# Kernel optimization log

Measured on AMD Instinct MI355X. Metric: run time of the kernel, lower is better.

Reference implementation:

```python
import jax, jax.numpy as jnp
import numpy as np

B, S, DIM, H = 4, 2048, 1024, 16
DEPTH = DIM // H


def setup_inputs() -> dict:
    key = jax.random.key(0)
    ks = jax.random.split(key, 12)
    s = 0.02
    return {
        "Q": jax.random.normal(ks[0], (B, S, DIM), jnp.float32),
        "K": jax.random.normal(ks[1], (B, S, DIM), jnp.float32),
        "V": jax.random.normal(ks[2], (B, S, DIM), jnp.float32),
        "mask": jax.random.randint(ks[3], (B, 1, 1, S), 0, 2).astype(jnp.float32),
        "Wq": jax.random.normal(ks[4], (DIM, DIM), jnp.float32) * s,
        "bq": jnp.zeros((DIM,), jnp.float32),
        "Wk": jax.random.normal(ks[5], (DIM, DIM), jnp.float32) * s,
        "bk": jnp.zeros((DIM,), jnp.float32),
        "Wv": jax.random.normal(ks[6], (DIM, DIM), jnp.float32) * s,
        "bv": jnp.zeros((DIM,), jnp.float32),
        "Wo": jax.random.normal(ks[7], (DIM, DIM), jnp.float32) * s,
        "bo": jnp.zeros((DIM,), jnp.float32),
    }


def _split_heads(x):
    # [B,S,DIM] -> [B,H,S,DEPTH]
    return x.reshape(x.shape[0], x.shape[1], H, DEPTH).transpose(0, 2, 1, 3)


def reference(Q, K, V, mask, Wq, bq, Wk, bk, Wv, bv, Wo, bo):
    q = _split_heads(Q @ Wq + bq)
    k = _split_heads(K @ Wk + bk)
    v = _split_heads(V @ Wv + bv)
    # scaled dot-product attention; note original scales by sqrt(depth) = last dim of K after split
    logits = jnp.einsum("bhqd,bhkd->bhqk", q, k) / jnp.sqrt(jnp.float32(DEPTH))
    logits = logits + mask * -1e9
    attn = jax.nn.softmax(logits, axis=-1)
    ctx = jnp.einsum("bhqk,bhkd->bhqd", attn, v)
    ctx = ctx.transpose(0, 2, 1, 3).reshape(Q.shape[0], Q.shape[1], DIM)
    return ctx @ Wo + bo
```

## Files before the change

### kernel.cpp

```cpp
#include <hip/hip_runtime.h>

typedef short s16x8 __attribute__((ext_vector_type(8)));
typedef short s16x4 __attribute__((ext_vector_type(4)));
typedef float f32x4 __attribute__((ext_vector_type(4)));

#define MFMA32(a, b, c) __builtin_amdgcn_mfma_f32_16x16x32_bf16((a), (b), (c), 0, 0, 0)

__device__ __forceinline__ void stage16(const unsigned short* g, unsigned short* l) {
#if defined(__HIP_DEVICE_COMPILE__)
  __builtin_amdgcn_global_load_lds((const __attribute__((address_space(1))) unsigned int*)g,
                                   (__attribute__((address_space(3))) unsigned int*)l, 16, 0, 0);
#endif
}

__device__ __forceinline__ unsigned short f2b(float f) {
  unsigned int u = __builtin_bit_cast(unsigned int, f);
  unsigned int r = u + 0x7FFFu + ((u >> 16) & 1u);
  return (unsigned short)(r >> 16);
}
__device__ __forceinline__ unsigned int pk2(float a, float b) {
#if defined(__HIP_DEVICE_COMPILE__)
  unsigned int ua = __builtin_bit_cast(unsigned int, a);
  unsigned int ub = __builtin_bit_cast(unsigned int, b);
  ua += 0x7FFFu + ((ua >> 16) & 1u);
  ub += 0x7FFFu + ((ub >> 16) & 1u);
  return __builtin_amdgcn_perm(ub, ua, 0x07060302u);
#else
  return (unsigned int)f2b(a) | ((unsigned int)f2b(b) << 16);
#endif
}
__device__ __forceinline__ float fast_exp2(float x) {
#if defined(__HIP_DEVICE_COMPILE__) && __has_builtin(__builtin_amdgcn_exp2f)
  return __builtin_amdgcn_exp2f(x);
#else
  return exp2f(x);
#endif
}

__global__ void wtrans(const float* __restrict__ W0, const float* __restrict__ W1,
                       const float* __restrict__ W2, const float* __restrict__ W3,
                       unsigned short* __restrict__ T0, unsigned short* __restrict__ T1,
                       unsigned short* __restrict__ T2, unsigned short* __restrict__ T3) {
  const float* W;
  unsigned short* T;
  switch (blockIdx.z) {
    case 0: W = W0; T = T0; break;
    case 1: W = W1; T = T1; break;
    case 2: W = W2; T = T2; break;
    default: W = W3; T = T3; break;
  }
  __shared__ float tile[32][33];
  const int n0 = blockIdx.x << 5;
  const int k0 = blockIdx.y << 5;
  const int tx = threadIdx.x;
  const int ty = threadIdx.y;
#pragma unroll
  for (int j = 0; j < 4; ++j)
    tile[ty + 8 * j][tx] = W[(size_t)(k0 + ty + 8 * j) * 1024 + n0 + tx];
  __syncthreads();
#pragma unroll
  for (int j = 0; j < 4; ++j)
    T[(size_t)(n0 + ty + 8 * j) * 1024 + k0 + tx] = f2b(tile[tx][ty + 8 * j]);
}

__global__ __launch_bounds__(256, 3) void gemm_qkv(
    const float* __restrict__ Qf, const float* __restrict__ Kf, const float* __restrict__ Vf,
    const unsigned short* __restrict__ Wqt, const unsigned short* __restrict__ Wkt,
    const unsigned short* __restrict__ Wvt, const float* __restrict__ bq,
    const float* __restrict__ bk, const float* __restrict__ bv,
    unsigned short* __restrict__ qh, unsigned short* __restrict__ kh,
    unsigned short* __restrict__ vtb, float qscale) {
  const int lid = blockIdx.x + (blockIdx.y << 3) + (blockIdx.z << 9);
  const int xcd = lid & 7;
  const int s = lid >> 3;
  const int tx = s & 7;
  const int g = ((s >> 3) << 3) | xcd;
  const int ty = g & 63;
  const int tz = g >> 6;

  const float* A;
  const unsigned short* Bt;
  const float* bias;
  unsigned short* Cout;
  float oscale = 1.0f;
  int vmode = 0;
  switch (tz) {
    case 0: A = Qf; Bt = Wqt; bias = bq; Cout = qh; oscale = qscale; break;
    case 1: A = Kf; Bt = Wkt; bias = bk; Cout = kh; break;
    default: A = Vf; Bt = Wvt; bias = bv; Cout = vtb; vmode = 1; break;
  }
  __shared__ __align__(16) unsigned short As[2 * 128 * 32];
  __shared__ __align__(16) unsigned short Bs[2 * 128 * 32];
  const int n0 = tx * 128;
  const int m0 = ty * 128;
  const int tid = threadIdx.x;
  const int w = tid >> 6;
  const int lane = tid & 63;
  const int lr = lane & 15;
  const int lg = lane >> 4;
  const int wm = (w >> 1) << 6;
  const int wn = (w & 1) << 6;

  const int srow = w * 16 + (lane >> 2);
  const int sseg = lane & 3;
  const float* Ag0 = A + (size_t)(m0 + srow) * 1024 + sseg * 8;
  const float* Ag1 = A + (size_t)(m0 + 64 + srow) * 1024 + sseg * 8;
  const unsigned short* Bg0 = Bt + (size_t)(n0 + srow) * 1024 + sseg * 8;
  const unsigned short* Bg1 = Bt + (size_t)(n0 + 64 + srow) * 1024 + sseg * 8;
  unsigned short* Bl0 = &Bs[(w * 16) * 32];
  unsigned short* Bl1 = &Bs[(64 + w * 16) * 32];
  const int aoff0 = (w * 16) * 32 + lane * 8;
  const int aoff1 = (64 + w * 16) * 32 + lane * 8;

  f32x4 acc[4][4];
#pragma unroll
  for (int i = 0; i < 4; ++i)
#pragma unroll
    for (int j = 0; j < 4; ++j) {
      f32x4 z = {0.f, 0.f, 0.f, 0.f};
      acc[i][j] = z;
    }

  {
    float4 a0lo = *(const float4*)Ag0;
    float4 a0hi = *(const float4*)(Ag0 + 4);
    float4 a1lo = *(const float4*)Ag1;
    float4 a1hi = *(const float4*)(Ag1 + 4);
    stage16(Bg0, Bl0);
    stage16(Bg1, Bl1);
    uint4 u0, u1;
    u0.x = pk2(a0lo.x, a0lo.y); u0.y = pk2(a0lo.z, a0lo.w);
    u0.z = pk2(a0hi.x, a0hi.y); u0.w = pk2(a0hi.z, a0hi.w);
    u1.x = pk2(a1lo.x, a1lo.y); u1.y = pk2(a1lo.z, a1lo.w);
    u1.z = pk2(a1hi.x, a1hi.y); u1.w = pk2(a1hi.z, a1hi.w);
    *(uint4*)&As[aoff0] = u0;
    *(uint4*)&As[aoff1] = u1;
  }
  asm volatile("s_waitcnt vmcnt(0) lgkmcnt(0)\n\ts_barrier" ::: "memory");

  int cur = 0;
  for (int k0 = 0; k0 < 1024; k0 += 32) {
    const bool next = (k0 + 32) < 1024;
    float4 a0lo, a0hi, a1lo, a1hi;
    if (next) {
      a0lo = *(const float4*)(Ag0 + k0 + 32);
      a0hi = *(const float4*)(Ag0 + k0 + 36);
      a1lo = *(const float4*)(Ag1 + k0 + 32);
      a1hi = *(const float4*)(Ag1 + k0 + 36);
      const int nb = (cur ^ 1) * 4096;
      stage16(Bg0 + k0 + 32, Bl0 + nb);
      stage16(Bg1 + k0 + 32, Bl1 + nb);
    }
    const int cb = cur * 4096;
    s16x8 af[4], bfr[4];
#pragma unroll
    for (int mt = 0; mt < 4; ++mt)
      af[mt] = *(const s16x8*)&As[cb + (wm + mt * 16 + lr) * 32 + lg * 8];
#pragma unroll
    for (int nt = 0; nt < 4; ++nt)
      bfr[nt] = *(const s16x8*)&Bs[cb + (wn + nt * 16 + lr) * 32 + lg * 8];
#pragma unroll
    for (int mt = 0; mt < 4; ++mt)
#pragma unroll
      for (int nt = 0; nt < 4; ++nt)
        acc[mt][nt] = MFMA32(af[mt], bfr[nt], acc[mt][nt]);
    if (next) {
      const int nb = (cur ^ 1) * 4096;
      uint4 u0, u1;
      u0.x = pk2(a0lo.x, a0lo.y); u0.y = pk2(a0lo.z, a0lo.w);
      u0.z = pk2(a0hi.x, a0hi.y); u0.w = pk2(a0hi.z, a0hi.w);
      u1.x = pk2(a1lo.x, a1lo.y); u1.y = pk2(a1lo.z, a1lo.w);
      u1.z = pk2(a1hi.x, a1hi.y); u1.w = pk2(a1hi.z, a1hi.w);
      *(uint4*)&As[nb + aoff0] = u0;
      *(uint4*)&As[nb + aoff1] = u1;
    }
    asm volatile("s_waitcnt vmcnt(0) lgkmcnt(0)\n\ts_barrier" ::: "memory");
    cur ^= 1;
  }

  float bcol[4];
#pragma unroll
  for (int nt = 0; nt < 4; ++nt) bcol[nt] = bias[n0 + wn + nt * 16 + lr];

  if (vmode == 0) {
#pragma unroll
    for (int mt = 0; mt < 4; ++mt)
#pragma unroll
      for (int nt = 0; nt < 4; ++nt)
#pragma unroll
        for (int r = 0; r < 4; ++r) {
          float v = (acc[mt][nt][r] + bcol[nt]) * oscale;
          int row = m0 + wm + mt * 16 + lg * 4 + r;
          int col = n0 + wn + nt * 16 + lr;
          int b = row >> 11, ss = row & 2047, hh = col >> 6, d = col & 63;
          Cout[(((size_t)(b * 16 + hh) * 2048 + ss) << 6) + d] = f2b(v);
        }
  } else {
#pragma unroll
    for (int mt = 0; mt < 4; ++mt)
#pragma unroll
      for (int nt = 0; nt < 4; ++nt)
#pragma unroll
        for (int r = 0; r < 4; ++r) {
          float v = acc[mt][nt][r] + bcol[nt];
          int row = m0 + wm + mt * 16 + lg * 4 + r;
          int col = n0 + wn + nt * 16 + lr;
          int b = row >> 11, ss = row & 2047, hh = col >> 6, d = col & 63;
          Cout[(((size_t)(b * 16 + hh) * 64 + d) << 11) + ss] = f2b(v);
        }
  }
}

__global__ __launch_bounds__(256, 3) void gemm_out(const unsigned short* __restrict__ A,
                                                   const unsigned short* __restrict__ Bt,
                                                   const float* __restrict__ bias,
                                                   float* __restrict__ Cout) {
  const int lid = blockIdx.x + (blockIdx.y << 3);
  const int xcd = lid & 7;
  const int s = lid >> 3;
  const int tx = s & 7;
  const int ty = ((s >> 3) << 3) | xcd;

  __shared__ __align__(16) unsigned short As[2 * 128 * 32];
  __shared__ __align__(16) unsigned short Bs[2 * 128 * 32];
  const int n0 = tx * 128;
  const int m0 = ty * 128;
  const int tid = threadIdx.x;
  const int w = tid >> 6;
  const int lane = tid & 63;
  const int lr = lane & 15;
  const int lg = lane >> 4;
  const int wm = (w >> 1) << 6;
  const int wn = (w & 1) << 6;

  const int srow = w * 16 + (lane >> 2);
  const int sseg = lane & 3;
  const unsigned short* Ag0 = A + (size_t)(m0 + srow) * 1024 + sseg * 8;
  const unsigned short* Ag1 = A + (size_t)(m0 + 64 + srow) * 1024 + sseg * 8;
  const unsigned short* Bg0 = Bt + (size_t)(n0 + srow) * 1024 + sseg * 8;
  const unsigned short* Bg1 = Bt + (size_t)(n0 + 64 + srow) * 1024 + sseg * 8;
  unsigned short* Al0 = &As[(w * 16) * 32];
  unsigned short* Al1 = &As[(64 + w * 16) * 32];
  unsigned short* Bl0 = &Bs[(w * 16) * 32];
  unsigned short* Bl1 = &Bs[(64 + w * 16) * 32];

  f32x4 acc[4][4];
#pragma unroll
  for (int i = 0; i < 4; ++i)
#pragma unroll
    for (int j = 0; j < 4; ++j) {
      f32x4 z = {0.f, 0.f, 0.f, 0.f};
      acc[i][j] = z;
    }

  stage16(Ag0, Al0);
  stage16(Ag1, Al1);
  stage16(Bg0, Bl0);
  stage16(Bg1, Bl1);
  asm volatile("s_waitcnt vmcnt(0)\n\ts_barrier" ::: "memory");

  int cur = 0;
  for (int k0 = 0; k0 < 1024; k0 += 32) {
    if (k0 + 32 < 1024) {
      const int nb = (cur ^ 1) * 4096;
      stage16(Ag0 + k0 + 32, Al0 + nb);
      stage16(Ag1 + k0 + 32, Al1 + nb);
      stage16(Bg0 + k0 + 32, Bl0 + nb);
      stage16(Bg1 + k0 + 32, Bl1 + nb);
    }
    const int cb = cur * 4096;
    s16x8 af[4], bfr[4];
#pragma unroll
    for (int mt = 0; mt < 4; ++mt)
      af[mt] = *(const s16x8*)&As[cb + (wm + mt * 16 + lr) * 32 + lg * 8];
#pragma unroll
    for (int nt = 0; nt < 4; ++nt)
      bfr[nt] = *(const s16x8*)&Bs[cb + (wn + nt * 16 + lr) * 32 + lg * 8];
#pragma unroll
    for (int mt = 0; mt < 4; ++mt)
#pragma unroll
      for (int nt = 0; nt < 4; ++nt)
        acc[mt][nt] = MFMA32(af[mt], bfr[nt], acc[mt][nt]);
    asm volatile("s_waitcnt vmcnt(0)\n\ts_barrier" ::: "memory");
    cur ^= 1;
  }

  float bcol[4];
#pragma unroll
  for (int nt = 0; nt < 4; ++nt) bcol[nt] = bias[n0 + wn + nt * 16 + lr];

#pragma unroll
  for (int mt = 0; mt < 4; ++mt)
#pragma unroll
    for (int nt = 0; nt < 4; ++nt)
#pragma unroll
      for (int r = 0; r < 4; ++r) {
        float v = acc[mt][nt][r] + bcol[nt];
        int row = m0 + wm + mt * 16 + lg * 4 + r;
        int col = n0 + wn + nt * 16 + lr;
        Cout[(size_t)row * 1024 + col] = v;
      }
}

__global__ __launch_bounds__(256, 4) void flash_attn(const unsigned short* __restrict__ qh,
                                                     const unsigned short* __restrict__ kh,
                                                     const unsigned short* __restrict__ vt,
                                                     const float* __restrict__ mask,
                                                     unsigned short* __restrict__ ctx) {
  const float c2 = 1.4426950408889634e9f;
  const int id = blockIdx.x;
  const int bh = id & 63;
  const int qtile = id >> 6;
  const int b = bh >> 4;
  const int h = bh & 15;
  const int q0 = qtile << 7;
  const int tid = threadIdx.x;
  const int w = tid >> 6;
  const int lane = tid & 63;
  const int lr = lane & 15;
  const int lg = lane >> 4;

  __shared__ __align__(16) unsigned short Ks[2 * 64 * 64];
  __shared__ __align__(16) unsigned short Vs[2 * 64 * 64];

  const unsigned short* qbase = qh + ((size_t)bh * 2048 + q0 + w * 32) * 64;
  const unsigned short* kbase = kh + (size_t)bh * 2048 * 64;
  const unsigned short* vbase = vt + (size_t)bh * 64 * 2048;
  const float* mbase = mask + b * 2048;

  const int rowc = lane >> 3;
  const int gseg = (lane & 7) ^ rowc;
  const unsigned short* kg0 = kbase + (size_t)(w * 16 + rowc) * 64 + gseg * 8;
  const unsigned short* kg1 = kbase + (size_t)(w * 16 + 8 + rowc) * 64 + gseg * 8;
  const unsigned short* vg0 = vbase + (size_t)(w * 16 + rowc) * 2048 + gseg * 8;
  const unsigned short* vg1 = vbase + (size_t)(w * 16 + 8 + rowc) * 2048 + gseg * 8;
  unsigned short* kl0 = &Ks[(w * 16 + 0) * 64];
  unsigned short* kl1 = &Ks[(w * 16 + 8) * 64];
  unsigned short* vl0 = &Vs[(w * 16 + 0) * 64];
  unsigned short* vl1 = &Vs[(w * 16 + 8) * 64];

  s16x8 qf[2][2];
#pragma unroll
  for (int qt = 0; qt < 2; ++qt)
#pragma unroll
    for (int kk = 0; kk < 2; ++kk)
      qf[qt][kk] = *(const s16x8*)(qbase + (qt * 16 + lr) * 64 + kk * 32 + lg * 8);

  const s16x8 ones8 = {(short)0x3F80, (short)0x3F80, (short)0x3F80, (short)0x3F80,
                       (short)0x3F80, (short)0x3F80, (short)0x3F80, (short)0x3F80};

  f32x4 o_acc[2][4];
  f32x4 l_acc[2];
#pragma unroll
  for (int qt = 0; qt < 2; ++qt) {
    f32x4 z = {0.f, 0.f, 0.f, 0.f};
    l_acc[qt] = z;
#pragma unroll
    for (int dt = 0; dt < 4; ++dt) o_acc[qt][dt] = z;
  }

  stage16(kg0, kl0);
  stage16(kg1, kl1);
  stage16(vg0, vl0);
  stage16(vg1, vl1);
  asm volatile("s_waitcnt vmcnt(0)\n\ts_barrier" ::: "memory");

  int cur = 0;
  for (int t0 = 0; t0 < 2048; t0 += 64) {
    if (t0 + 64 < 2048) {
      const int nb = (cur ^ 1) * 4096;
      stage16(kg0 + (size_t)(t0 + 64) * 64, kl0 + nb);
      stage16(kg1 + (size_t)(t0 + 64) * 64, kl1 + nb);
      stage16(vg0 + (t0 + 64), vl0 + nb);
      stage16(vg1 + (t0 + 64), vl1 + nb);
    }
    float4 mk[4];
#pragma unroll
    for (int kt = 0; kt < 4; ++kt) mk[kt] = *(const float4*)(mbase + t0 + kt * 16 + lg * 4);

    const int cb = cur * 4096;
    const int sw = lr & 7;
    unsigned int pw[4][2][2];
#pragma unroll
    for (int kt = 0; kt < 4; ++kt) {
      const int krow = kt * 16 + lr;
      s16x8 kf0 = *(const s16x8*)&Ks[cb + krow * 64 + ((lg ^ sw) * 8)];
      s16x8 kf1 = *(const s16x8*)&Ks[cb + krow * 64 + (((4 + lg) ^ sw) * 8)];
      float ml0 = mk[kt].x * c2, ml1 = mk[kt].y * c2;
      float ml2 = mk[kt].z * c2, ml3 = mk[kt].w * c2;
#pragma unroll
      for (int qt = 0; qt < 2; ++qt) {
        f32x4 s = {0.f, 0.f, 0.f, 0.f};
        s = MFMA32(kf0, qf[qt][0], s);
        s = MFMA32(kf1, qf[qt][1], s);
        pw[kt][qt][0] = pk2(fast_exp2(s[0] - ml0), fast_exp2(s[1] - ml1));
        pw[kt][qt][1] = pk2(fast_exp2(s[2] - ml2), fast_exp2(s[3] - ml3));
      }
    }

#pragma unroll
    for (int c = 0; c < 2; ++c) {
      s16x8 pb[2];
#pragma unroll
      for (int qt = 0; qt < 2; ++qt) {
        uint4 u;
        u.x = pw[2 * c][qt][0];
        u.y = pw[2 * c][qt][1];
        u.z = pw[2 * c + 1][qt][0];
        u.w = pw[2 * c + 1][qt][1];
        pb[qt] = __builtin_bit_cast(s16x8, u);
        l_acc[qt] = MFMA32(ones8, pb[qt], l_acc[qt]);
      }
      const int plo = ((c << 2) | (lg >> 1)) ^ sw;
      const int phi = ((c << 2) | 2 | (lg >> 1)) ^ sw;
      const int sub = (lg & 1) * 4;
#pragma unroll
      for (int dt = 0; dt < 4; ++dt) {
        const int d = dt * 16 + lr;
        s16x4 vlo = *(const s16x4*)&Vs[cb + d * 64 + plo * 8 + sub];
        s16x4 vhi = *(const s16x4*)&Vs[cb + d * 64 + phi * 8 + sub];
        s16x8 vf = __builtin_shufflevector(vlo, vhi, 0, 1, 2, 3, 4, 5, 6, 7);
#pragma unroll
        for (int qt = 0; qt < 2; ++qt) o_acc[qt][dt] = MFMA32(vf, pb[qt], o_acc[qt][dt]);
      }
    }

    asm volatile("s_waitcnt vmcnt(0)\n\ts_barrier" ::: "memory");
    cur ^= 1;
  }

#pragma unroll
  for (int qt = 0; qt < 2; ++qt) {
    float inv = 1.0f / l_acc[qt][0];
    int q = q0 + w * 32 + qt * 16 + lr;
    unsigned short* cp = ctx + ((size_t)(b * 2048 + q) * 16 + h) * 64 + lg * 4;
#pragma unroll
    for (int dt = 0; dt < 4; ++dt) {
      f32x4 o = o_acc[qt][dt];
      uint2 u;
      u.x = pk2(o[0] * inv, o[1] * inv);
      u.y = pk2(o[2] * inv, o[3] * inv);
      *(uint2*)(cp + dt * 16) = u;
    }
  }
}

extern "C" void kernel_launch(void* const* d_in, const int* in_sizes, int n_in,
                              void* d_out, int out_size, void* d_ws, size_t ws_size,
                              hipStream_t stream) {
  (void)in_sizes; (void)n_in; (void)out_size; (void)ws_size;
  const float* Q = (const float*)d_in[0];
  const float* K = (const float*)d_in[1];
  const float* V = (const float*)d_in[2];
  const float* mask = (const float*)d_in[3];
  const float* Wq = (const float*)d_in[4];
  const float* bq = (const float*)d_in[5];
  const float* Wk = (const float*)d_in[6];
  const float* bk = (const float*)d_in[7];
  const float* Wv = (const float*)d_in[8];
  const float* bv = (const float*)d_in[9];
  const float* Wo = (const float*)d_in[10];
  const float* bo = (const float*)d_in[11];

  char* ws = (char*)d_ws;
  unsigned short* wqt = (unsigned short*)(ws + (size_t)0);
  unsigned short* wkt = (unsigned short*)(ws + ((size_t)2 << 20));
  unsigned short* wvt = (unsigned short*)(ws + ((size_t)4 << 20));
  unsigned short* wot = (unsigned short*)(ws + ((size_t)6 << 20));
  unsigned short* qhb = (unsigned short*)(ws + ((size_t)8 << 20));
  unsigned short* khb = (unsigned short*)(ws + ((size_t)24 << 20));
  unsigned short* vtb = (unsigned short*)(ws + ((size_t)40 << 20));
  unsigned short* ctx = (unsigned short*)(ws + ((size_t)56 << 20));

  wtrans<<<dim3(32, 32, 4), dim3(32, 8), 0, stream>>>(Wq, Wk, Wv, Wo, wqt, wkt, wvt, wot);

  const float qscale = 0.18033688011112042f;

  gemm_qkv<<<dim3(8, 64, 3), dim3(256), 0, stream>>>(Q, K, V, wqt, wkt, wvt, bq, bk, bv,
                                                     qhb, khb, vtb, qscale);

  flash_attn<<<dim3(1024), dim3(256), 0, stream>>>(qhb, khb, vtb, mask, ctx);

  gemm_out<<<dim3(8, 64), dim3(256), 0, stream>>>(ctx, wot, bo, (float*)d_out);
}
```

Before: 368.5 us.

## Triple-buffer LDS staging in projection GEMMs with two-deep prefetch

```diff
diff --git a/kernel.cpp b/kernel.cpp
--- a/kernel.cpp
+++ b/kernel.cpp
@@ -72,9 +72,9 @@
     unsigned short* __restrict__ vtb, float qscale) {
   const int lid = blockIdx.x + (blockIdx.y << 3) + (blockIdx.z << 9);
   const int xcd = lid & 7;
-  const int s = lid >> 3;
-  const int tx = s & 7;
-  const int g = ((s >> 3) << 3) | xcd;
+  const int sl = lid >> 3;
+  const int tx = sl & 7;
+  const int g = ((sl >> 3) << 3) | xcd;
   const int ty = g & 63;
   const int tz = g >> 6;
 
@@ -89,8 +89,8 @@
     case 1: A = Kf; Bt = Wkt; bias = bk; Cout = kh; break;
     default: A = Vf; Bt = Wvt; bias = bv; Cout = vtb; vmode = 1; break;
   }
-  __shared__ __align__(16) unsigned short As[2 * 128 * 32];
-  __shared__ __align__(16) unsigned short Bs[2 * 128 * 32];
+  __shared__ __align__(16) unsigned short As[3 * 128 * 32];
+  __shared__ __align__(16) unsigned short Bs[3 * 128 * 32];
   const int n0 = tx * 128;
   const int m0 = ty * 128;
   const int tid = threadIdx.x;
@@ -107,8 +107,10 @@
   const float* Ag1 = A + (size_t)(m0 + 64 + srow) * 1024 + sseg * 8;
   const unsigned short* Bg0 = Bt + (size_t)(n0 + srow) * 1024 + sseg * 8;
   const unsigned short* Bg1 = Bt + (size_t)(n0 + 64 + srow) * 1024 + sseg * 8;
-  unsigned short* Bl0 = &Bs[(w * 16) * 32];
-  unsigned short* Bl1 = &Bs[(64 + w * 16) * 32];
+  unsigned short *ab0 = &As[0], *ab1 = &As[4096], *ab2 = &As[8192];
+  unsigned short *bb0 = &Bs[0], *bb1 = &Bs[4096], *bb2 = &Bs[8192];
+  const int bl0 = (w * 16) * 32;
+  const int bl1 = (64 + w * 16) * 32;
   const int aoff0 = (w * 16) * 32 + lane * 8;
   const int aoff1 = (64 + w * 16) * 32 + lane * 8;
 
@@ -121,61 +123,68 @@
       acc[i][j] = z;
     }
 
+  float4 pa0lo, pa0hi, pa1lo, pa1hi;
+
+  stage16(Bg0, bb0 + bl0);
+  stage16(Bg1, bb0 + bl1);
+  stage16(Bg0 + 32, bb1 + bl0);
+  stage16(Bg1 + 32, bb1 + bl1);
+  pa0lo = *(const float4*)Ag0;
+  pa0hi = *(const float4*)(Ag0 + 4);
+  pa1lo = *(const float4*)Ag1;
+  pa1hi = *(const float4*)(Ag1 + 4);
   {
-    float4 a0lo = *(const float4*)Ag0;
-    float4 a0hi = *(const float4*)(Ag0 + 4);
-    float4 a1lo = *(const float4*)Ag1;
-    float4 a1hi = *(const float4*)(Ag1 + 4);
-    stage16(Bg0, Bl0);
-    stage16(Bg1, Bl1);
     uint4 u0, u1;
-    u0.x = pk2(a0lo.x, a0lo.y); u0.y = pk2(a0lo.z, a0lo.w);
-    u0.z = pk2(a0hi.x, a0hi.y); u0.w = pk2(a0hi.z, a0hi.w);
-    u1.x = pk2(a1lo.x, a1lo.y); u1.y = pk2(a1lo.z, a1lo.w);
-    u1.z = pk2(a1hi.x, a1hi.y); u1.w = pk2(a1hi.z, a1hi.w);
-    *(uint4*)&As[aoff0] = u0;
-    *(uint4*)&As[aoff1] = u1;
-  }
-  asm volatile("s_waitcnt vmcnt(0) lgkmcnt(0)\n\ts_barrier" ::: "memory");
-
-  int cur = 0;
-  for (int k0 = 0; k0 < 1024; k0 += 32) {
-    const bool next = (k0 + 32) < 1024;
-    float4 a0lo, a0hi, a1lo, a1hi;
-    if (next) {
-      a0lo = *(const float4*)(Ag0 + k0 + 32);
-      a0hi = *(const float4*)(Ag0 + k0 + 36);
-      a1lo = *(const float4*)(Ag1 + k0 + 32);
-      a1hi = *(const float4*)(Ag1 + k0 + 36);
-      const int nb = (cur ^ 1) * 4096;
-      stage16(Bg0 + k0 + 32, Bl0 + nb);
-      stage16(Bg1 + k0 + 32, Bl1 + nb);
-    }
-    const int cb = cur * 4096;
+    u0.x = pk2(pa0lo.x, pa0lo.y); u0.y = pk2(pa0lo.z, pa0lo.w);
+    u0.z = pk2(pa0hi.x, pa0hi.y); u0.w = pk2(pa0hi.z, pa0hi.w);
+    u1.x = pk2(pa1lo.x, pa1lo.y); u1.y = pk2(pa1lo.z, pa1lo.w);
+    u1.z = pk2(pa1hi.x, pa1hi.y); u1.w = pk2(pa1hi.z, pa1hi.w);
+    *(uint4*)&ab0[aoff0] = u0;
+    *(uint4*)&ab0[aoff1] = u1;
+  }
+  pa0lo = *(const float4*)(Ag0 + 32);
+  pa0hi = *(const float4*)(Ag0 + 36);
+  pa1lo = *(const float4*)(Ag1 + 32);
+  pa1hi = *(const float4*)(Ag1 + 36);
+  asm volatile("s_waitcnt lgkmcnt(0)\n\ts_barrier" ::: "memory");
+
+  for (int i = 0; i < 32; ++i) {
+    const int k2 = (i + 2) * 32;
+    if (i + 2 < 32) {
+      stage16(Bg0 + k2, bb2 + bl0);
+      stage16(Bg1 + k2, bb2 + bl1);
+    }
     s16x8 af[4], bfr[4];
 #pragma unroll
     for (int mt = 0; mt < 4; ++mt)
-      af[mt] = *(const s16x8*)&As[cb + (wm + mt * 16 + lr) * 32 + lg * 8];
+      af[mt] = *(const s16x8*)&ab0[(wm + mt * 16 + lr) * 32 + lg * 8];
 #pragma unroll
     for (int nt = 0; nt < 4; ++nt)
-      bfr[nt] = *(const s16x8*)&Bs[cb + (wn + nt * 16 + lr) * 32 + lg * 8];
+      bfr[nt] = *(const s16x8*)&bb0[(wn + nt * 16 + lr) * 32 + lg * 8];
 #pragma unroll
     for (int mt = 0; mt < 4; ++mt)
 #pragma unroll
       for (int nt = 0; nt < 4; ++nt)
         acc[mt][nt] = MFMA32(af[mt], bfr[nt], acc[mt][nt]);
-    if (next) {
-      const int nb = (cur ^ 1) * 4096;
+    if (i + 1 < 32) {
       uint4 u0, u1;
-      u0.x = pk2(a0lo.x, a0lo.y); u0.y = pk2(a0lo.z, a0lo.w);
-      u0.z = pk2(a0hi.x, a0hi.y); u0.w = pk2(a0hi.z, a0hi.w);
-      u1.x = pk2(a1lo.x, a1lo.y); u1.y = pk2(a1lo.z, a1lo.w);
-      u1.z = pk2(a1hi.x, a1hi.y); u1.w = pk2(a1hi.z, a1hi.w);
-      *(uint4*)&As[nb + aoff0] = u0;
-      *(uint4*)&As[nb + aoff1] = u1;
-    }
-    asm volatile("s_waitcnt vmcnt(0) lgkmcnt(0)\n\ts_barrier" ::: "memory");
-    cur ^= 1;
+      u0.x = pk2(pa0lo.x, pa0lo.y); u0.y = pk2(pa0lo.z, pa0lo.w);
+      u0.z = pk2(pa0hi.x, pa0hi.y); u0.w = pk2(pa0hi.z, pa0hi.w);
+      u1.x = pk2(pa1lo.x, pa1lo.y); u1.y = pk2(pa1lo.z, pa1lo.w);
+      u1.z = pk2(pa1hi.x, pa1hi.y); u1.w = pk2(pa1hi.z, pa1hi.w);
+      *(uint4*)&ab1[aoff0] = u0;
+      *(uint4*)&ab1[aoff1] = u1;
+    }
+    if (i + 2 < 32) {
+      pa0lo = *(const float4*)(Ag0 + k2);
+      pa0hi = *(const float4*)(Ag0 + k2 + 4);
+      pa1lo = *(const float4*)(Ag1 + k2);
+      pa1hi = *(const float4*)(Ag1 + k2 + 4);
+    }
+    asm volatile("s_waitcnt vmcnt(6) lgkmcnt(0)\n\ts_barrier" ::: "memory");
+    unsigned short* t;
+    t = ab0; ab0 = ab1; ab1 = ab2; ab2 = t;
+    t = bb0; bb0 = bb1; bb1 = bb2; bb2 = t;
   }
 
   float bcol[4];
@@ -217,12 +226,12 @@
                                                    float* __restrict__ Cout) {
   const int lid = blockIdx.x + (blockIdx.y << 3);
   const int xcd = lid & 7;
-  const int s = lid >> 3;
-  const int tx = s & 7;
-  const int ty = ((s >> 3) << 3) | xcd;
-
-  __shared__ __align__(16) unsigned short As[2 * 128 * 32];
-  __shared__ __align__(16) unsigned short Bs[2 * 128 * 32];
+  const int sl = lid >> 3;
+  const int tx = sl & 7;
+  const int ty = ((sl >> 3) << 3) | xcd;
+
+  __shared__ __align__(16) unsigned short As[3 * 128 * 32];
+  __shared__ __align__(16) unsigned short Bs[3 * 128 * 32];
   const int n0 = tx * 128;
   const int m0 = ty * 128;
   const int tid = threadIdx.x;
@@ -239,10 +248,10 @@
   const unsigned short* Ag1 = A + (size_t)(m0 + 64 + srow) * 1024 + sseg * 8;
   const unsigned short* Bg0 = Bt + (size_t)(n0 + srow) * 1024 + sseg * 8;
   const unsigned short* Bg1 = Bt + (size_t)(n0 + 64 + srow) * 1024 + sseg * 8;
-  unsigned short* Al0 = &As[(w * 16) * 32];
-  unsigned short* Al1 = &As[(64 + w * 16) * 32];
-  unsigned short* Bl0 = &Bs[(w * 16) * 32];
-  unsigned short* Bl1 = &Bs[(64 + w * 16) * 32];
+  unsigned short *ab0 = &As[0], *ab1 = &As[4096], *ab2 = &As[8192];
+  unsigned short *bb0 = &Bs[0], *bb1 = &Bs[4096], *bb2 = &Bs[8192];
+  const int hl0 = (w * 16) * 32;
+  const int hl1 = (64 + w * 16) * 32;
 
   f32x4 acc[4][4];
 #pragma unroll
@@ -253,36 +262,40 @@
       acc[i][j] = z;
     }
 
-  stage16(Ag0, Al0);
-  stage16(Ag1, Al1);
-  stage16(Bg0, Bl0);
-  stage16(Bg1, Bl1);
-  asm volatile("s_waitcnt vmcnt(0)\n\ts_barrier" ::: "memory");
-
-  int cur = 0;
-  for (int k0 = 0; k0 < 1024; k0 += 32) {
-    if (k0 + 32 < 1024) {
-      const int nb = (cur ^ 1) * 4096;
-      stage16(Ag0 + k0 + 32, Al0 + nb);
-      stage16(Ag1 + k0 + 32, Al1 + nb);
-      stage16(Bg0 + k0 + 32, Bl0 + nb);
-      stage16(Bg1 + k0 + 32, Bl1 + nb);
-    }
-    const int cb = cur * 4096;
+  stage16(Ag0, ab0 + hl0);
+  stage16(Ag1, ab0 + hl1);
+  stage16(Bg0, bb0 + hl0);
+  stage16(Bg1, bb0 + hl1);
+  stage16(Ag0 + 32, ab1 + hl0);
+  stage16(Ag1 + 32, ab1 + hl1);
+  stage16(Bg0 + 32, bb1 + hl0);
+  stage16(Bg1 + 32, bb1 + hl1);
+  asm volatile("s_waitcnt vmcnt(4)\n\ts_barrier" ::: "memory");
+
+  for (int i = 0; i < 32; ++i) {
+    const int k2 = (i + 2) * 32;
+    if (i + 2 < 32) {
+      stage16(Ag0 + k2, ab2 + hl0);
+      stage16(Ag1 + k2, ab2 + hl1);
+      stage16(Bg0 + k2, bb2 + hl0);
+      stage16(Bg1 + k2, bb2 + hl1);
+    }
     s16x8 af[4], bfr[4];
 #pragma unroll
     for (int mt = 0; mt < 4; ++mt)
-      af[mt] = *(const s16x8*)&As[cb + (wm + mt * 16 + lr) * 32 + lg * 8];
+      af[mt] = *(const s16x8*)&ab0[(wm + mt * 16 + lr) * 32 + lg * 8];
 #pragma unroll
     for (int nt = 0; nt < 4; ++nt)
-      bfr[nt] = *(const s16x8*)&Bs[cb + (wn + nt * 16 + lr) * 32 + lg * 8];
+      bfr[nt] = *(const s16x8*)&bb0[(wn + nt * 16 + lr) * 32 + lg * 8];
 #pragma unroll
     for (int mt = 0; mt < 4; ++mt)
 #pragma unroll
       for (int nt = 0; nt < 4; ++nt)
         acc[mt][nt] = MFMA32(af[mt], bfr[nt], acc[mt][nt]);
-    asm volatile("s_waitcnt vmcnt(0)\n\ts_barrier" ::: "memory");
-    cur ^= 1;
+    asm volatile("s_waitcnt vmcnt(4)\n\ts_barrier" ::: "memory");
+    unsigned short* t;
+    t = ab0; ab0 = ab1; ab1 = ab2; ab2 = t;
+    t = bb0; bb0 = bb1; bb1 = bb2; bb2 = t;
   }
 
   float bcol[4];
```

Result: no change. 361.7 us (-1.8%).
